# Optimization experiments

Hardware: AMD Instinct MI355X
Metric: run time of the kernel (lower is better)

## Reference

```python
import math
import jax, jax.numpy as jnp
import numpy as np

TAR_MIN, TAR_MAX = 0.0, 1.0
SRC_MIN, SRC_MAX = 0.0, 1.0
NUM_BINS_TAR = 32
NUM_BINS_SRC = 32
SIGMA_TAR = 0.5 * (TAR_MAX - TAR_MIN) / NUM_BINS_TAR
SIGMA_SRC = 0.5 * (SRC_MAX - SRC_MIN) / NUM_BINS_SRC
EPS = 1e-10


def setup_inputs() -> dict:
    key = jax.random.key(0)
    k1, k2 = jax.random.split(key)
    shape = (4, 1, 96, 96, 96)
    tar = jax.random.uniform(k1, shape, dtype=jnp.float32)
    src = jax.random.uniform(k2, shape, dtype=jnp.float32)
    return {"tar": tar, "src": src}


def _minmax_normalise(x, min_out, max_out):
    # per-sample minmax over all non-batch dims; x: (N, P)
    mn = jnp.min(x, axis=1, keepdims=True)
    mx = jnp.max(x, axis=1, keepdims=True)
    return (x - mn) / (mx - mn + 1e-12) * (max_out - min_out) + min_out


def _window(x, bins, sigma):
    # x: (N, P); bins: (B,) -> (N, B, P) Gaussian soft-binning
    d = x[:, None, :] - bins[None, :, None]
    return jnp.exp(-(d * d) / (2.0 * sigma * sigma)) / math.sqrt(2.0 * math.pi) * sigma


def reference(tar, src):
    N = tar.shape[0]
    t = tar[:, 0].reshape(N, -1)  # (N, P)
    s = src[:, 0].reshape(N, -1)
    t = _minmax_normalise(t, TAR_MIN, TAR_MAX)
    s = _minmax_normalise(s, SRC_MIN, SRC_MAX)

    bins_tar = jnp.linspace(TAR_MIN, TAR_MAX, NUM_BINS_TAR, dtype=t.dtype)
    bins_src = jnp.linspace(SRC_MIN, SRC_MAX, NUM_BINS_SRC, dtype=s.dtype)

    wt = _window(t, bins_tar, SIGMA_TAR)  # (N, Bt, P)
    ws = _window(s, bins_src, SIGMA_SRC)  # (N, Bs, P)

    hist_joint = jnp.einsum('bip,bjp->bij', wt, ws)  # (N, Bt, Bs)
    hist_norm = jnp.sum(hist_joint, axis=(1, 2), keepdims=True)
    p_joint = hist_joint / hist_norm

    p_tar = jnp.sum(p_joint, axis=2)  # (N, Bt)
    p_src = jnp.sum(p_joint, axis=1)  # (N, Bs)

    ent_tar = -jnp.sum(p_tar * jnp.log(p_tar + EPS), axis=1)
    ent_src = -jnp.sum(p_src * jnp.log(p_src + EPS), axis=1)
    ent_joint = -jnp.sum(p_joint * jnp.log(p_joint + EPS), axis=(1, 2))

    # normalised=True
    return -jnp.mean((ent_tar + ent_src) / ent_joint)
```

## Files before the change

kernel.cpp:

```cpp
#include <hip/hip_runtime.h>
#include <math.h>

#define N_SAMPLES 4
#define P_ELEMS   (96*96*96)
#define MM_BPS    216
#define MM_T4     1024
#define H_BPS     432
#define H_TILE    2048
#define H_T4      (H_TILE/4)
#define NCOPY     8
#define WS        1.75343855f
#define EPSR      1e-10f

typedef __attribute__((ext_vector_type(8)))  short short8;
typedef __attribute__((ext_vector_type(16))) float float16;

#define PW_COUNT  (N_SAMPLES * H_BPS)


__global__ void __launch_bounds__(256)
k_minmax(const float* __restrict__ tar, const float* __restrict__ src,
         float4* __restrict__ pw, float* __restrict__ histall) {
    __shared__ float4 sred[4];
    int n = blockIdx.y, j = blockIdx.x;
    int t = threadIdx.x;
    const float4* t4 = (const float4*)(tar + (size_t)n * P_ELEMS) + (size_t)j * MM_T4;
    const float4* s4 = (const float4*)(src + (size_t)n * P_ELEMS) + (size_t)j * MM_T4;
    float4 a0 = t4[t], a1 = t4[t + 256], a2 = t4[t + 512], a3 = t4[t + 768];
    float4 b0 = s4[t], b1 = s4[t + 256], b2 = s4[t + 512], b3 = s4[t + 768];
    float mnt = fminf(fminf(fminf(a0.x, a0.y), fminf(a0.z, a0.w)),
                      fminf(fminf(a1.x, a1.y), fminf(a1.z, a1.w)));
    mnt = fminf(mnt, fminf(fminf(fminf(a2.x, a2.y), fminf(a2.z, a2.w)),
                           fminf(fminf(a3.x, a3.y), fminf(a3.z, a3.w))));
    float mxt = fmaxf(fmaxf(fmaxf(a0.x, a0.y), fmaxf(a0.z, a0.w)),
                      fmaxf(fmaxf(a1.x, a1.y), fmaxf(a1.z, a1.w)));
    mxt = fmaxf(mxt, fmaxf(fmaxf(fmaxf(a2.x, a2.y), fmaxf(a2.z, a2.w)),
                           fmaxf(fmaxf(a3.x, a3.y), fmaxf(a3.z, a3.w))));
    float mns = fminf(fminf(fminf(b0.x, b0.y), fminf(b0.z, b0.w)),
                      fminf(fminf(b1.x, b1.y), fminf(b1.z, b1.w)));
    mns = fminf(mns, fminf(fminf(fminf(b2.x, b2.y), fminf(b2.z, b2.w)),
                           fminf(fminf(b3.x, b3.y), fminf(b3.z, b3.w))));
    float mxs = fmaxf(fmaxf(fmaxf(b0.x, b0.y), fmaxf(b0.z, b0.w)),
                      fmaxf(fmaxf(b1.x, b1.y), fmaxf(b1.z, b1.w)));
    mxs = fmaxf(mxs, fmaxf(fmaxf(fmaxf(b2.x, b2.y), fmaxf(b2.z, b2.w)),
                           fmaxf(fmaxf(b3.x, b3.y), fmaxf(b3.z, b3.w))));
    #pragma unroll
    for (int o = 32; o; o >>= 1) {
        mnt = fminf(mnt, __shfl_xor(mnt, o));
        mxt = fmaxf(mxt, __shfl_xor(mxt, o));
        mns = fminf(mns, __shfl_xor(mns, o));
        mxs = fmaxf(mxs, __shfl_xor(mxs, o));
    }
    int lane = t & 63, wave = t >> 6;
    if (lane == 0) sred[wave] = make_float4(mnt, mxt, mns, mxs);
    __syncthreads();
    if (t == 0) {
        float4 v0 = sred[0], v1 = sred[1], v2 = sred[2], v3 = sred[3];
        float4 r;
        r.x = fminf(fminf(v0.x, v1.x), fminf(v2.x, v3.x));
        r.y = fmaxf(fmaxf(v0.y, v1.y), fmaxf(v2.y, v3.y));
        r.z = fminf(fminf(v0.z, v1.z), fminf(v2.z, v3.z));
        r.w = fmaxf(fmaxf(v0.w, v1.w), fmaxf(v2.w, v3.w));
        pw[n * MM_BPS + j] = r;
    }
    int bid = n * MM_BPS + j;
    if (bid < 128) histall[bid * 256 + t] = 0.0f;
}


__global__ void __launch_bounds__(256, 8)
k_hist(const float* __restrict__ tar, const float* __restrict__ src,
       const float4* __restrict__ pw, float* __restrict__ histall) {
    __shared__ __align__(16) float lds[2 * H_TILE];
    __shared__ float4 sred[4];
    __shared__ float bc[4];
    int n = blockIdx.y, j = blockIdx.x;
    int t = threadIdx.x;

    const float4* t4 = (const float4*)(tar + (size_t)n * P_ELEMS) + (size_t)j * H_T4;
    const float4* s4 = (const float4*)(src + (size_t)n * P_ELEMS) + (size_t)j * H_T4;
    float4 a0 = t4[t], a1 = t4[t + 256];
    float4 b0 = s4[t], b1 = s4[t + 256];

    {
        const float4* pwn = pw + n * MM_BPS;
        float mnt = INFINITY, mxt = -INFINITY, mns = INFINITY, mxs = -INFINITY;
        if (t < MM_BPS) {
            float4 v = pwn[t];
            mnt = v.x; mxt = v.y; mns = v.z; mxs = v.w;
        }
        #pragma unroll
        for (int o = 32; o; o >>= 1) {
            mnt = fminf(mnt, __shfl_xor(mnt, o));
            mxt = fmaxf(mxt, __shfl_xor(mxt, o));
            mns = fminf(mns, __shfl_xor(mns, o));
            mxs = fmaxf(mxs, __shfl_xor(mxs, o));
        }
        int lane = t & 63, wave = t >> 6;
        if (lane == 0) sred[wave] = make_float4(mnt, mxt, mns, mxs);
        __syncthreads();
        if (t == 0) {
            float4 v0 = sred[0], v1 = sred[1], v2 = sred[2], v3 = sred[3];
            bc[0] = fminf(fminf(v0.x, v1.x), fminf(v2.x, v3.x));
            bc[1] = fmaxf(fmaxf(v0.y, v1.y), fmaxf(v2.y, v3.y));
            bc[2] = fminf(fminf(v0.z, v1.z), fminf(v2.z, v3.z));
            bc[3] = fmaxf(fmaxf(v0.w, v1.w), fmaxf(v2.w, v3.w));
        }
        __syncthreads();
    }
    float mnt = bc[0], mns = bc[2];
    float fit = 31.0f * WS / (bc[1] - mnt + 1e-12f);
    float fis = 31.0f * WS / (bc[3] - mns + 1e-12f);

    {
        float4 xo, yo;
        xo.x = (a0.x - mnt) * fit; xo.y = (a0.y - mnt) * fit;
        xo.z = (a0.z - mnt) * fit; xo.w = (a0.w - mnt) * fit;
        ((float4*)lds)[t] = xo;
        xo.x = (a1.x - mnt) * fit; xo.y = (a1.y - mnt) * fit;
        xo.z = (a1.z - mnt) * fit; xo.w = (a1.w - mnt) * fit;
        ((float4*)lds)[t + 256] = xo;
        yo.x = (b0.x - mns) * fis; yo.y = (b0.y - mns) * fis;
        yo.z = (b0.z - mns) * fis; yo.w = (b0.w - mns) * fis;
        ((float4*)(lds + H_TILE))[t] = yo;
        yo.x = (b1.x - mns) * fis; yo.y = (b1.y - mns) * fis;
        yo.z = (b1.z - mns) * fis; yo.w = (b1.w - mns) * fis;
        ((float4*)(lds + H_TILE))[t + 256] = yo;
    }
    __syncthreads();

    int lane = t & 63, wave = t >> 6, g = lane >> 5;
    float q = (float)(lane & 31) * WS;
    const float* xb = lds + wave * (H_TILE / 4);
    const float* yb = lds + H_TILE + wave * (H_TILE / 4);

    float16 acc;
    #pragma unroll
    for (int i = 0; i < 16; i++) acc[i] = 0.0f;

    #pragma unroll 4
    for (int it = 0; it < H_TILE / 4 / 16; it++) {
        int kb = it * 16 + g * 8;
        float4 xa = *(const float4*)(xb + kb);
        float4 xc = *(const float4*)(xb + kb + 4);
        float4 ya = *(const float4*)(yb + kb);
        float4 yc = *(const float4*)(yb + kb + 4);
        float xs[8] = {xa.x, xa.y, xa.z, xa.w, xc.x, xc.y, xc.z, xc.w};
        float ys[8] = {ya.x, ya.y, ya.z, ya.w, yc.x, yc.y, yc.z, yc.w};
        unsigned av[8], bv[8];
        #pragma unroll
        for (int jj = 0; jj < 8; jj++) {
            float d = xs[jj] - q;
            float arg = -d * d;
            float w;
            asm("v_exp_f32 %0, %1" : "=v"(w) : "v"(arg));
            av[jj] = __float_as_uint(w);
            d = ys[jj] - q;
            arg = -d * d;
            asm("v_exp_f32 %0, %1" : "=v"(w) : "v"(arg));
            bv[jj] = __float_as_uint(w);
        }
        union { unsigned u[4]; short8 v; } af, bf;
        #pragma unroll
        for (int jj = 0; jj < 4; jj++) {
            af.u[jj] = __builtin_amdgcn_perm(av[2 * jj + 1], av[2 * jj], 0x07060302u);
            bf.u[jj] = __builtin_amdgcn_perm(bv[2 * jj + 1], bv[2 * jj], 0x07060302u);
        }
        acc = __builtin_amdgcn_mfma_f32_32x32x16_bf16(af.v, bf.v, acc, 0, 0, 0);
    }

    __syncthreads();
    {
        float* hw = lds + wave * 1024;
        int col = lane & 31;
        #pragma unroll
        for (int reg = 0; reg < 16; reg++) {
            int row = (reg & 3) + 8 * (reg >> 2) + 4 * g;
            hw[row * 32 + col] = acc[reg];
        }
    }
    __syncthreads();
    float* histn = histall + ((j & (NCOPY - 1)) * N_SAMPLES + n) * 1024;
    for (int bb = t; bb < 1024; bb += 256) {
        float v = lds[bb] + lds[1024 + bb] + lds[2048 + bb] + lds[3072 + bb];
        unsafeAtomicAdd(&histn[bb], v);
    }
}


__global__ void __launch_bounds__(256)
k_final(const float* __restrict__ histall, float* __restrict__ out) {
    __shared__ float sh[4096];
    __shared__ float wres[4];
    int t = threadIdx.x;
    int lane = t & 63, nn = t >> 6;
    float4 h[4];
    float part = 0.0f;
    #pragma unroll
    for (int r = 0; r < 4; r++) {
        float4 s = make_float4(0.f, 0.f, 0.f, 0.f);
        #pragma unroll
        for (int c = 0; c < NCOPY; c++) {
            const float4* h4 = (const float4*)(histall + (c * N_SAMPLES + nn) * 1024);
            float4 v = h4[lane * 4 + r];
            s.x += v.x; s.y += v.y; s.z += v.z; s.w += v.w;
        }
        h[r] = s;
        part += (s.x + s.y) + (s.z + s.w);
    }
    #pragma unroll
    for (int o = 32; o; o >>= 1) part += __shfl_xor(part, o);
    float inv = 1.0f / part;
    float ej = 0.0f;
    #pragma unroll
    for (int r = 0; r < 4; r++) {
        float4 p;
        p.x = h[r].x * inv; p.y = h[r].y * inv; p.z = h[r].z * inv; p.w = h[r].w * inv;
        ((float4*)(sh + nn * 1024))[lane * 4 + r] = p;
        ej -= p.x * __logf(p.x + EPSR) + p.y * __logf(p.y + EPSR)
            + p.z * __logf(p.z + EPSR) + p.w * __logf(p.w + EPSR);
    }
    #pragma unroll
    for (int o = 32; o; o >>= 1) ej += __shfl_xor(ej, o);
    __syncthreads();
    float m = 0.0f;
    if (lane < 32) {
        int row = lane;
        for (int jj = 0; jj < 32; jj++) m += sh[nn * 1024 + row * 32 + ((jj + row) & 31)];
    } else {
        int col = lane - 32;
        for (int i = 0; i < 32; i++) m += sh[nn * 1024 + i * 32 + col];
    }
    float rc = -m * __logf(m + EPSR);
    #pragma unroll
    for (int o = 16; o; o >>= 1) rc += __shfl_xor(rc, o);
    float es = __shfl(rc, 32);
    if (lane == 0) wres[nn] = (rc + es) / ej;
    __syncthreads();
    if (t == 0)
        out[0] = -(wres[0] + wres[1] + wres[2] + wres[3]) * 0.25f;
}

extern "C" void kernel_launch(void* const* d_in, const int* in_sizes, int n_in,
                              void* d_out, int out_size, void* d_ws, size_t ws_size,
                              hipStream_t stream) {
    const float* tar = (const float*)d_in[0];
    const float* src = (const float*)d_in[1];
    float* out = (float*)d_out;
    float4* pw = (float4*)d_ws;
    float* histall = (float*)((char*)d_ws + PW_COUNT * 16);

    k_minmax<<<dim3(MM_BPS, N_SAMPLES), 256, 0, stream>>>(tar, src, pw, histall);
    k_hist<<<dim3(H_BPS, N_SAMPLES), 256, 0, stream>>>(tar, src, pw, histall);
    k_final<<<1, 256, 0, stream>>>(histall, out);
}
```

Measured before the change: 110.6 us.

## Fuse minmax, histogram and final entropy into one kernel with grid barrier

Merges the three kernels into one persistent-style kernel. Each block keeps its 4096-element tile in registers across a spin-wait grid barrier on an atomic counter, so inputs are read once instead of twice. The last block to finish, detected by a second counter, computes the entropies. This removes two launches and the re-read of the inputs. In exchange it depends on all 864 blocks being co-resident to avoid deadlock, and halves the block count, which lowers occupancy in the MFMA phase.

```diff
diff --git a/kernel.cpp b/kernel.cpp
--- a/kernel.cpp
+++ b/kernel.cpp
@@ -1,33 +1,55 @@
 #include <hip/hip_runtime.h>
 #include <math.h>
 
-#define N_SAMPLES 4
+#define NS        4
 #define P_ELEMS   (96*96*96)
-#define MM_BPS    216
-#define MM_T4     1024
-#define H_BPS     432
-#define H_TILE    2048
-#define H_T4      (H_TILE/4)
+#define BPS       216
+#define TILE      4096
 #define NCOPY     8
+#define NBLOCKS   (NS*BPS)
 #define WS        1.75343855f
 #define EPSR      1e-10f
 
 typedef __attribute__((ext_vector_type(8)))  short short8;
 typedef __attribute__((ext_vector_type(16))) float float16;
 
-#define PW_COUNT  (N_SAMPLES * H_BPS)
-
-
-__global__ void __launch_bounds__(256)
-k_minmax(const float* __restrict__ tar, const float* __restrict__ src,
-         float4* __restrict__ pw, float* __restrict__ histall) {
+#define SCOPE_AGENT __HIP_MEMORY_SCOPE_AGENT
+
+__device__ __forceinline__ float aload(const float* p) {
+    return __hip_atomic_load(p, __ATOMIC_RELAXED, SCOPE_AGENT);
+}
+__device__ __forceinline__ void astore(float* p, float v) {
+    __hip_atomic_store(p, v, __ATOMIC_RELAXED, SCOPE_AGENT);
+}
+
+
+__global__ void k_zero(unsigned* __restrict__ counterA) {
+    if (threadIdx.x == 0)
+        __hip_atomic_store(counterA, 0u, __ATOMIC_RELAXED, SCOPE_AGENT);
+}
+
+__global__ void __launch_bounds__(256, 4)
+k_fused(const float* __restrict__ tar, const float* __restrict__ src,
+        float* __restrict__ pw4, float* __restrict__ histall,
+        unsigned* __restrict__ counterA, unsigned* __restrict__ counterB,
+        float* __restrict__ out)
+{
+    __shared__ __align__(16) float lds[2 * TILE];
     __shared__ float4 sred[4];
-    int n = blockIdx.y, j = blockIdx.x;
-    int t = threadIdx.x;
-    const float4* t4 = (const float4*)(tar + (size_t)n * P_ELEMS) + (size_t)j * MM_T4;
-    const float4* s4 = (const float4*)(src + (size_t)n * P_ELEMS) + (size_t)j * MM_T4;
+    __shared__ float bc[4];
+    __shared__ float wres[4];
+    __shared__ int lastflag;
+
+    const int n = blockIdx.y, j = blockIdx.x;
+    const int t = threadIdx.x;
+    const int bid = n * BPS + j;
+    const int lane = t & 63, wave = t >> 6;
+
+    const float4* t4 = (const float4*)(tar + (size_t)n * P_ELEMS) + (size_t)j * (TILE / 4);
+    const float4* s4 = (const float4*)(src + (size_t)n * P_ELEMS) + (size_t)j * (TILE / 4);
     float4 a0 = t4[t], a1 = t4[t + 256], a2 = t4[t + 512], a3 = t4[t + 768];
     float4 b0 = s4[t], b1 = s4[t + 256], b2 = s4[t + 512], b3 = s4[t + 768];
+
     float mnt = fminf(fminf(fminf(a0.x, a0.y), fminf(a0.z, a0.w)),
                       fminf(fminf(a1.x, a1.y), fminf(a1.z, a1.w)));
     mnt = fminf(mnt, fminf(fminf(fminf(a2.x, a2.y), fminf(a2.z, a2.w)),
@@ -51,53 +73,41 @@
         mns = fminf(mns, __shfl_xor(mns, o));
         mxs = fmaxf(mxs, __shfl_xor(mxs, o));
     }
-    int lane = t & 63, wave = t >> 6;
     if (lane == 0) sred[wave] = make_float4(mnt, mxt, mns, mxs);
     __syncthreads();
     if (t == 0) {
         float4 v0 = sred[0], v1 = sred[1], v2 = sred[2], v3 = sred[3];
-        float4 r;
-        r.x = fminf(fminf(v0.x, v1.x), fminf(v2.x, v3.x));
-        r.y = fmaxf(fmaxf(v0.y, v1.y), fmaxf(v2.y, v3.y));
-        r.z = fminf(fminf(v0.z, v1.z), fminf(v2.z, v3.z));
-        r.w = fmaxf(fmaxf(v0.w, v1.w), fmaxf(v2.w, v3.w));
-        pw[n * MM_BPS + j] = r;
-    }
-    int bid = n * MM_BPS + j;
-    if (bid < 128) histall[bid * 256 + t] = 0.0f;
-}
-
-
-__global__ void __launch_bounds__(256, 8)
-k_hist(const float* __restrict__ tar, const float* __restrict__ src,
-       const float4* __restrict__ pw, float* __restrict__ histall) {
-    __shared__ __align__(16) float lds[2 * H_TILE];
-    __shared__ float4 sred[4];
-    __shared__ float bc[4];
-    int n = blockIdx.y, j = blockIdx.x;
-    int t = threadIdx.x;
-
-    const float4* t4 = (const float4*)(tar + (size_t)n * P_ELEMS) + (size_t)j * H_T4;
-    const float4* s4 = (const float4*)(src + (size_t)n * P_ELEMS) + (size_t)j * H_T4;
-    float4 a0 = t4[t], a1 = t4[t + 256];
-    float4 b0 = s4[t], b1 = s4[t + 256];
-
-    {
-        const float4* pwn = pw + n * MM_BPS;
-        float mnt = INFINITY, mxt = -INFINITY, mns = INFINITY, mxs = -INFINITY;
-        if (t < MM_BPS) {
-            float4 v = pwn[t];
-            mnt = v.x; mxt = v.y; mns = v.z; mxs = v.w;
+        astore(&pw4[bid * 4 + 0], fminf(fminf(v0.x, v1.x), fminf(v2.x, v3.x)));
+        astore(&pw4[bid * 4 + 1], fmaxf(fmaxf(v0.y, v1.y), fmaxf(v2.y, v3.y)));
+        astore(&pw4[bid * 4 + 2], fminf(fminf(v0.z, v1.z), fminf(v2.z, v3.z)));
+        astore(&pw4[bid * 4 + 3], fmaxf(fmaxf(v0.w, v1.w), fmaxf(v2.w, v3.w)));
+    }
+    if (bid < 129) astore(&histall[bid * 256 + t], 0.0f);
+
+    __syncthreads();
+    if (t == 0) {
+        __threadfence();
+        __hip_atomic_fetch_add(counterA, 1u, __ATOMIC_RELEASE, SCOPE_AGENT);
+        while (__hip_atomic_load(counterA, __ATOMIC_ACQUIRE, SCOPE_AGENT) < NBLOCKS)
+            __builtin_amdgcn_s_sleep(2);
+    }
+    __syncthreads();
+
+    {
+        float rmnt = INFINITY, rmxt = -INFINITY, rmns = INFINITY, rmxs = -INFINITY;
+        if (t < BPS) {
+            const float* p = pw4 + (n * BPS + t) * 4;
+            rmnt = aload(p + 0); rmxt = aload(p + 1);
+            rmns = aload(p + 2); rmxs = aload(p + 3);
         }
         #pragma unroll
         for (int o = 32; o; o >>= 1) {
-            mnt = fminf(mnt, __shfl_xor(mnt, o));
-            mxt = fmaxf(mxt, __shfl_xor(mxt, o));
-            mns = fminf(mns, __shfl_xor(mns, o));
-            mxs = fmaxf(mxs, __shfl_xor(mxs, o));
-        }
-        int lane = t & 63, wave = t >> 6;
-        if (lane == 0) sred[wave] = make_float4(mnt, mxt, mns, mxs);
+            rmnt = fminf(rmnt, __shfl_xor(rmnt, o));
+            rmxt = fmaxf(rmxt, __shfl_xor(rmxt, o));
+            rmns = fminf(rmns, __shfl_xor(rmns, o));
+            rmxs = fmaxf(rmxs, __shfl_xor(rmxs, o));
+        }
+        if (lane == 0) sred[wave] = make_float4(rmnt, rmxt, rmns, rmxs);
         __syncthreads();
         if (t == 0) {
             float4 v0 = sred[0], v1 = sred[1], v2 = sred[2], v3 = sred[3];
@@ -108,38 +118,42 @@
         }
         __syncthreads();
     }
-    float mnt = bc[0], mns = bc[2];
-    float fit = 31.0f * WS / (bc[1] - mnt + 1e-12f);
-    float fis = 31.0f * WS / (bc[3] - mns + 1e-12f);
-
-    {
-        float4 xo, yo;
-        xo.x = (a0.x - mnt) * fit; xo.y = (a0.y - mnt) * fit;
-        xo.z = (a0.z - mnt) * fit; xo.w = (a0.w - mnt) * fit;
-        ((float4*)lds)[t] = xo;
-        xo.x = (a1.x - mnt) * fit; xo.y = (a1.y - mnt) * fit;
-        xo.z = (a1.z - mnt) * fit; xo.w = (a1.w - mnt) * fit;
-        ((float4*)lds)[t + 256] = xo;
-        yo.x = (b0.x - mns) * fis; yo.y = (b0.y - mns) * fis;
-        yo.z = (b0.z - mns) * fis; yo.w = (b0.w - mns) * fis;
-        ((float4*)(lds + H_TILE))[t] = yo;
-        yo.x = (b1.x - mns) * fis; yo.y = (b1.y - mns) * fis;
-        yo.z = (b1.z - mns) * fis; yo.w = (b1.w - mns) * fis;
-        ((float4*)(lds + H_TILE))[t + 256] = yo;
-    }
-    __syncthreads();
-
-    int lane = t & 63, wave = t >> 6, g = lane >> 5;
-    float q = (float)(lane & 31) * WS;
-    const float* xb = lds + wave * (H_TILE / 4);
-    const float* yb = lds + H_TILE + wave * (H_TILE / 4);
+    float gmnt = bc[0], gmns = bc[2];
+    float fit = 31.0f * WS / (bc[1] - gmnt + 1e-12f);
+    float fis = 31.0f * WS / (bc[3] - gmns + 1e-12f);
+
+    {
+        float4 v;
+        v.x=(a0.x-gmnt)*fit; v.y=(a0.y-gmnt)*fit; v.z=(a0.z-gmnt)*fit; v.w=(a0.w-gmnt)*fit;
+        ((float4*)lds)[t] = v;
+        v.x=(a1.x-gmnt)*fit; v.y=(a1.y-gmnt)*fit; v.z=(a1.z-gmnt)*fit; v.w=(a1.w-gmnt)*fit;
+        ((float4*)lds)[t + 256] = v;
+        v.x=(a2.x-gmnt)*fit; v.y=(a2.y-gmnt)*fit; v.z=(a2.z-gmnt)*fit; v.w=(a2.w-gmnt)*fit;
+        ((float4*)lds)[t + 512] = v;
+        v.x=(a3.x-gmnt)*fit; v.y=(a3.y-gmnt)*fit; v.z=(a3.z-gmnt)*fit; v.w=(a3.w-gmnt)*fit;
+        ((float4*)lds)[t + 768] = v;
+        v.x=(b0.x-gmns)*fis; v.y=(b0.y-gmns)*fis; v.z=(b0.z-gmns)*fis; v.w=(b0.w-gmns)*fis;
+        ((float4*)(lds + TILE))[t] = v;
+        v.x=(b1.x-gmns)*fis; v.y=(b1.y-gmns)*fis; v.z=(b1.z-gmns)*fis; v.w=(b1.w-gmns)*fis;
+        ((float4*)(lds + TILE))[t + 256] = v;
+        v.x=(b2.x-gmns)*fis; v.y=(b2.y-gmns)*fis; v.z=(b2.z-gmns)*fis; v.w=(b2.w-gmns)*fis;
+        ((float4*)(lds + TILE))[t + 512] = v;
+        v.x=(b3.x-gmns)*fis; v.y=(b3.y-gmns)*fis; v.z=(b3.z-gmns)*fis; v.w=(b3.w-gmns)*fis;
+        ((float4*)(lds + TILE))[t + 768] = v;
+    }
+    __syncthreads();
+
+    const int g = lane >> 5;
+    const float q = (float)(lane & 31) * WS;
+    const float* xb = lds + wave * (TILE / 4);
+    const float* yb = lds + TILE + wave * (TILE / 4);
 
     float16 acc;
     #pragma unroll
     for (int i = 0; i < 16; i++) acc[i] = 0.0f;
 
     #pragma unroll 4
-    for (int it = 0; it < H_TILE / 4 / 16; it++) {
+    for (int it = 0; it < TILE / 4 / 16; it++) {
         int kb = it * 16 + g * 8;
         float4 xa = *(const float4*)(xb + kb);
         float4 xc = *(const float4*)(xb + kb + 4);
@@ -180,20 +194,26 @@
         }
     }
     __syncthreads();
-    float* histn = histall + ((j & (NCOPY - 1)) * N_SAMPLES + n) * 1024;
-    for (int bb = t; bb < 1024; bb += 256) {
-        float v = lds[bb] + lds[1024 + bb] + lds[2048 + bb] + lds[3072 + bb];
-        unsafeAtomicAdd(&histn[bb], v);
-    }
-}
-
-
-__global__ void __launch_bounds__(256)
-k_final(const float* __restrict__ histall, float* __restrict__ out) {
-    __shared__ float sh[4096];
-    __shared__ float wres[4];
-    int t = threadIdx.x;
-    int lane = t & 63, nn = t >> 6;
+    {
+        float* histn = histall + ((j & (NCOPY - 1)) * NS + n) * 1024;
+        for (int bb = t; bb < 1024; bb += 256) {
+            float v = lds[bb] + lds[1024 + bb] + lds[2048 + bb] + lds[3072 + bb];
+            unsafeAtomicAdd(&histn[bb], v);
+        }
+    }
+
+    __threadfence();
+    __syncthreads();
+    if (t == 0) {
+        unsigned old = __hip_atomic_fetch_add(counterB, 1u, __ATOMIC_ACQ_REL,
+                                              SCOPE_AGENT);
+        lastflag = (old == NBLOCKS - 1);
+    }
+    __syncthreads();
+    if (!lastflag) return;
+
+    float* sh = lds;
+    int nn = wave;
     float4 h[4];
     float part = 0.0f;
     #pragma unroll
@@ -201,9 +221,9 @@
         float4 s = make_float4(0.f, 0.f, 0.f, 0.f);
         #pragma unroll
         for (int c = 0; c < NCOPY; c++) {
-            const float4* h4 = (const float4*)(histall + (c * N_SAMPLES + nn) * 1024);
-            float4 v = h4[lane * 4 + r];
-            s.x += v.x; s.y += v.y; s.z += v.z; s.w += v.w;
+            const float* hp = histall + (c * NS + nn) * 1024 + (lane * 4 + r) * 4;
+            s.x += aload(hp + 0); s.y += aload(hp + 1);
+            s.z += aload(hp + 2); s.w += aload(hp + 3);
         }
         h[r] = s;
         part += (s.x + s.y) + (s.z + s.w);
@@ -247,10 +267,12 @@
     const float* tar = (const float*)d_in[0];
     const float* src = (const float*)d_in[1];
     float* out = (float*)d_out;
-    float4* pw = (float4*)d_ws;
-    float* histall = (float*)((char*)d_ws + PW_COUNT * 16);
-
-    k_minmax<<<dim3(MM_BPS, N_SAMPLES), 256, 0, stream>>>(tar, src, pw, histall);
-    k_hist<<<dim3(H_BPS, N_SAMPLES), 256, 0, stream>>>(tar, src, pw, histall);
-    k_final<<<1, 256, 0, stream>>>(histall, out);
-}
+    float* histall = (float*)d_ws;
+    unsigned* counterB = (unsigned*)(histall + 32768);
+    unsigned* counterA = (unsigned*)(histall + 33024);
+    float* pw4 = histall + 33040;
+
+    k_zero<<<1, 64, 0, stream>>>(counterA);
+    k_fused<<<dim3(BPS, NS), 256, 0, stream>>>(tar, src, pw4, histall,
+                                               counterA, counterB, out);
+}
```

Result: slower. 262.8 us (+137.6%).
